# Performance work log

Measured on AMD Instinct MI355X. Metric: run time of the kernel, lower is better.

Reference implementation:

```python
import jax, jax.numpy as jnp
import numpy as np

NO_LANE = 90  # sentinel label meaning 'no lane'

def smooth_l1(x):
    ax = jnp.abs(x)
    return jnp.where(ax < 1.0, 0.5 * x * x, ax - 0.5)

def setup_inputs() -> dict:
    key = jax.random.key(0)
    ks = jax.random.split(key, 10)
    B, M, T, L, NL, P = 32768, 6, 30, 10, 10, 50
    cls_ = jax.random.normal(ks[0], (B, M), dtype=jnp.float32)
    reg = jax.random.normal(ks[1], (B, M, T, 2), dtype=jnp.float32) * 5.0
    lane_cls = jax.random.normal(ks[2], (B, L), dtype=jnp.float32)
    gt_preds = jax.random.normal(ks[3], (B, T, 2), dtype=jnp.float32) * 5.0
    rot = jax.random.normal(ks[4], (B, 2, 2), dtype=jnp.float32)
    orig = jax.random.normal(ks[5], (B, 2), dtype=jnp.float32)
    lane_feats = jax.random.normal(ks[6], (B, NL, P, 2), dtype=jnp.float32) * 5.0
    has_preds = jax.random.uniform(ks[7], (B, T)) < 0.8
    has_preds = has_preds.at[:, 0].set(True)  # ensure mask = max_last > 1.0 holds for every row
    lane_labels = jax.random.randint(ks[8], (B,), 0, L, dtype=jnp.int32)
    lane_labels = jnp.where(jax.random.uniform(ks[9], (B,)) < 0.05, NO_LANE, lane_labels)
    return dict(cls=cls_, reg=reg, lane_cls=lane_cls, gt_preds=gt_preds, rot=rot,
                orig=orig, lane_feats=lane_feats, has_preds=has_preds, lane_labels=lane_labels)

def reference(cls, reg, lane_cls, gt_preds, rot, orig, lane_feats, has_preds, lane_labels):
    B, M, T, _ = reg.shape
    rows = jnp.arange(B)
    hasf = has_preds.astype(jnp.float32)

    # last valid timestep per agent (argmax of has + tiny time ramp)
    last = hasf + 0.1 * jnp.arange(T, dtype=jnp.float32) / T
    last_idcs = jnp.argmax(last, axis=1)
    mask = jnp.max(last, axis=1) > 1.0  # [B], all True by construction
    maskf = mask.astype(jnp.float32)

    # endpoint distance per mode -> min mode selection
    end_reg = reg[rows, :, last_idcs]            # [B, M, 2]
    end_gt = gt_preds[rows, last_idcs]           # [B, 2]
    dist = jnp.sqrt(((end_reg - end_gt[:, None, :]) ** 2).sum(-1))  # [B, M]
    min_idcs = jnp.argmin(dist, axis=1)

    # classification target: mode with min total squared error
    cls_tar = jnp.argmin(((reg - gt_preds[:, None]) ** 2).sum(-1).sum(-1), axis=1)
    nll = -jnp.take_along_axis(jax.nn.log_softmax(cls, axis=-1), cls_tar[:, None], axis=1)[:, 0]
    cls_loss = (nll * maskf).sum() / jnp.maximum(maskf.sum(), 1.0)  # CE mean over masked rows

    reg_sel = reg[rows, min_idcs]                # [B, T, 2]
    w_reg = hasf * maskf[:, None]
    reg_loss = (smooth_l1(reg_sel - gt_preds) * w_reg[:, :, None]).sum()
    num_reg = w_reg.sum()

    # lane classification: per-sample CE * (label+1), skipping sentinel
    valid = lane_labels != NO_LANE
    validf = valid.astype(jnp.float32)
    lab_c = jnp.where(valid, lane_labels, 0)
    lane_nll = -jnp.take_along_axis(jax.nn.log_softmax(lane_cls, axis=-1), lab_c[:, None], axis=1)[:, 0]
    lane_cls_loss = (lane_nll * (lab_c.astype(jnp.float32) + 1.0) * validf).sum()
    num_lane_cls = validf.sum()

    # lane-offset loss: lane polyline in global frame, point-to-lane min distances
    lane_sel = lane_feats[rows, lab_c]           # [B, P, 2]
    lane_w = jnp.einsum('bpc,bcd->bpd', lane_sel, rot) + orig[:, None, :]
    d_reg = jnp.linalg.norm(lane_w[:, None, :, :] - reg_sel[:, :, None, :], axis=-1).min(-1)  # [B, T]
    d_gt = jnp.linalg.norm(lane_w[:, None, :, :] - gt_preds[:, :, None, :], axis=-1).min(-1)  # [B, T]
    diff = d_reg - d_gt
    check = (d_reg >= d_gt).astype(jnp.float32)
    per = (diff * check * hasf).sum(1) / jnp.maximum(hasf.sum(1), 1.0)  # mean over valid steps
    w_off = validf * maskf
    lane_off_loss = (per * w_off).sum()
    num_lane_off = w_off.sum()

    return jnp.stack([cls_loss, maskf.sum() * 0 + 1.0, reg_loss, num_reg,
                      lane_cls_loss, num_lane_cls, lane_off_loss, num_lane_off])
```

## Files before the change

### kernel.cpp

```cpp
#include <hip/hip_runtime.h>
#include <math.h>

#define NO_LANE 90
constexpr int Bt  = 32768;
constexpr int Mm  = 6;
constexpr int Tt  = 30;
constexpr int Ll  = 10;
constexpr int NLl = 10;
constexpr int Pp  = 50;

constexpr int BPB   = 8;
constexpr int NBLK  = Bt / BPB;
constexpr int NSLOT = 64;
constexpr int LPAD  = 104;

__device__ __forceinline__ float smoothl1(float x) {
    float ax = fabsf(x);
    return ax < 1.0f ? 0.5f * x * x : ax - 0.5f;
}

template <int CTRL>
__device__ __forceinline__ float dppf(float x) {
    return __int_as_float(__builtin_amdgcn_update_dpp(
        0, __float_as_int(x), CTRL, 0xF, 0xF, true));
}
__device__ __forceinline__ float sum8(float x) {
    x += dppf<0xB1>(x);
    x += dppf<0x4E>(x);
    x += dppf<0x141>(x);
    return x;
}
__device__ __forceinline__ float sum16(float x) {
    x = sum8(x);
    x += dppf<0x140>(x);
    return x;
}
__device__ __forceinline__ float sum32(float x) {
    x += __shfl_xor(x, 16);
    return sum16(x);
}
__device__ __forceinline__ float max8(float x) {
    x = fmaxf(x, dppf<0xB1>(x));
    x = fmaxf(x, dppf<0x4E>(x));
    x = fmaxf(x, dppf<0x141>(x));
    return x;
}
__device__ __forceinline__ float max16(float x) {
    x = max8(x);
    x = fmaxf(x, dppf<0x140>(x));
    return x;
}

__global__ __launch_bounds__(256) void pred_loss_main(
    const float* __restrict__ cls, const float* __restrict__ reg,
    const float* __restrict__ lane_cls, const float* __restrict__ gt,
    const float* __restrict__ rot, const float* __restrict__ orig,
    const float* __restrict__ lane_feats, const unsigned char* __restrict__ hp,
    const int* __restrict__ lane_labels, float* __restrict__ slots) {

    __shared__ __align__(16) float sLW[BPB][LPAD];
    __shared__ float sPart[BPB][8];

    const int tid = threadIdx.x;
    const int sb  = tid >> 5;
    const int l   = tid & 31;
    const int h   = (tid >> 5) & 1;
    const int b   = blockIdx.x * BPB + sb;

    unsigned int u = ((const unsigned int*)hp)[tid & 63];
    unsigned int s = (u & 0xFFu) + ((u >> 8) & 0xFFu) +
                     ((u >> 16) & 0xFFu) + (u >> 24);
#pragma unroll
    for (int o = 32; o; o >>= 1) s += __shfl_xor((int)s, o);
    const bool byte_fmt = (s > 100u && s < 2000u);

    bool has = false;
    if (l < Tt) {
        int idx = b * Tt + l;
        has = byte_fmt ? (hp[idx] != 0)
                       : (((const unsigned int*)hp)[idx] != 0u);
    }
    unsigned long long ball = __ballot(has);
    unsigned int mmask = (unsigned int)(ball >> (h * 32));
    int   last  = 31 - __clz((int)(mmask | 1u));
    float maskf = (mmask >> 1) ? 1.0f : 0.0f;
    float n_has = (float)__popc((int)mmask);
    float hasf  = has ? 1.0f : 0.0f;

    int   lab    = lane_labels[b];
    bool  valid  = (lab != NO_LANE);
    int   lab_c  = valid ? lab : 0;
    float validf = valid ? 1.0f : 0.0f;

    float gx = 0.f, gy = 0.f;
    float rx[Mm], ry[Mm];
#pragma unroll
    for (int m = 0; m < Mm; ++m) { rx[m] = 0.f; ry[m] = 0.f; }
    if (l < Tt) {
        float2 g = *(const float2*)(gt + (size_t)b * (Tt * 2) + 2 * l);
        gx = g.x; gy = g.y;
        const float* regb = reg + (size_t)b * (Mm * Tt * 2) + 2 * l;
#pragma unroll
        for (int m = 0; m < Mm; ++m) {
            float2 r = *(const float2*)(regb + m * (Tt * 2));
            rx[m] = r.x; ry[m] = r.y;
        }
    }

    float4 R = *(const float4*)(rot + (size_t)b * 4);
    float2 O = *(const float2*)(orig + (size_t)b * 2);
    if (l < 25) {
        float4 ls = ((const float4*)(lane_feats +
                     ((size_t)b * NLl + lab_c) * (Pp * 2)))[l];
        float4 lw;
        lw.x = ls.x * R.x + ls.y * R.z + O.x;
        lw.y = ls.x * R.y + ls.y * R.w + O.y;
        lw.z = ls.z * R.x + ls.w * R.z + O.x;
        lw.w = ls.z * R.y + ls.w * R.w + O.y;
        ((float4*)&sLW[sb][0])[l] = lw;
    }

    float cm = (l < Mm) ? cls[(size_t)b * Mm + l] : -INFINITY;
    float lc = (l < Ll) ? lane_cls[(size_t)b * Ll + l] : -INFINITY;

    float pm[Mm];
#pragma unroll
    for (int m = 0; m < Mm; ++m) {
        float dx = rx[m] - gx, dy = ry[m] - gy;
        pm[m] = sum32(dx * dx + dy * dy);
    }
    int cls_tar = 0;
    float bestc = pm[0];
#pragma unroll
    for (int m = 1; m < Mm; ++m)
        if (pm[m] < bestc) { bestc = pm[m]; cls_tar = m; }

    int mi_loc = 0;
    {
        float dx = rx[0] - gx, dy = ry[0] - gy;
        float bd = dx * dx + dy * dy;
#pragma unroll
        for (int m = 1; m < Mm; ++m) {
            float ex_ = rx[m] - gx, ey_ = ry[m] - gy;
            float d2 = ex_ * ex_ + ey_ * ey_;
            if (d2 < bd) { bd = d2; mi_loc = m; }
        }
    }
    int min_i = __shfl(mi_loc, last + h * 32);

    float rsx = rx[0], rsy = ry[0];
#pragma unroll
    for (int m = 1; m < Mm; ++m)
        if (min_i == m) { rsx = rx[m]; rsy = ry[m]; }

    float mx = max8(cm);
    float ex = sum8((l < Mm) ? __expf(cm - mx) : 0.f);
    float ctar = __shfl(cm, cls_tar + h * 32);
    float nll  = mx + __logf(ex) - ctar;

    float mx2 = max16(lc);
    float ex2 = sum16((l < Ll) ? __expf(lc - mx2) : 0.f);
    float ltar = __shfl(lc, lab_c + h * 32);
    float lnll = mx2 + __logf(ex2) - ltar;

    float regl = sum32((smoothl1(rsx - gx) + smoothl1(rsy - gy)) * hasf * maskf);

    float dminR = INFINITY, dminG = INFINITY;
    const float4* lw4 = (const float4*)&sLW[sb][0];
#pragma unroll
    for (int j = 0; j < 25; ++j) {
        float4 q = lw4[j];
        float ax0 = q.x - rsx, ay0 = q.y - rsy;
        float ax1 = q.z - rsx, ay1 = q.w - rsy;
        dminR = fminf(dminR, fminf(ax0 * ax0 + ay0 * ay0, ax1 * ax1 + ay1 * ay1));
        float bx0 = q.x - gx, by0 = q.y - gy;
        float bx1 = q.z - gx, by1 = q.w - gy;
        dminG = fminf(dminG, fminf(bx0 * bx0 + by0 * by0, bx1 * bx1 + by1 * by1));
    }
    float dr = sqrtf(dminR), dg = sqrtf(dminG);
    float pern = sum32((dr >= dg) ? (dr - dg) * hasf : 0.f);

    if (l == 0) {
        float per = pern / fmaxf(n_has, 1.0f);
        sPart[sb][0] = nll * maskf;
        sPart[sb][1] = maskf;
        sPart[sb][2] = regl;
        sPart[sb][3] = maskf * n_has;
        sPart[sb][4] = lnll * (float)(lab_c + 1) * validf;
        sPart[sb][5] = validf;
        sPart[sb][6] = per * validf * maskf;
        sPart[sb][7] = validf * maskf;
    }
    __syncthreads();

    if (tid < 8) {
        float sum = 0.f;
#pragma unroll
        for (int k = 0; k < BPB; ++k) sum += sPart[k][tid];
        atomicAdd(&slots[(size_t)(blockIdx.x & (NSLOT - 1)) * 16 + tid], sum);
    }
}

__global__ __launch_bounds__(64) void finalize_k(const float* __restrict__ slots,
                                                 float* __restrict__ out) {
    int lane = threadIdx.x;
    int c  = lane & 7;
    int s0 = lane >> 3;
    float t = 0.f;
#pragma unroll
    for (int k = 0; k < 8; ++k)
        t += slots[(size_t)(s0 + k * 8) * 16 + c];
    t += __shfl_xor(t, 8);
    t += __shfl_xor(t, 16);
    t += __shfl_xor(t, 32);
    float r1 = __shfl(t, 1);
    if (lane == 0)      out[0] = t / fmaxf(r1, 1.0f);
    else if (lane == 1) out[1] = 1.0f;
    else if (lane < 8)  out[lane] = t;
}

extern "C" void kernel_launch(void* const* d_in, const int* in_sizes, int n_in,
                              void* d_out, int out_size, void* d_ws, size_t ws_size,
                              hipStream_t stream) {
    const float* cls        = (const float*)d_in[0];
    const float* reg        = (const float*)d_in[1];
    const float* lane_cls   = (const float*)d_in[2];
    const float* gt         = (const float*)d_in[3];
    const float* rot        = (const float*)d_in[4];
    const float* orig       = (const float*)d_in[5];
    const float* lane_feats = (const float*)d_in[6];
    const unsigned char* hp = (const unsigned char*)d_in[7];
    const int* lane_labels  = (const int*)d_in[8];
    float* out = (float*)d_out;

    float* slots = (float*)((char*)d_ws + 64);

    hipMemsetAsync(d_ws, 0, 64 + NSLOT * 16 * sizeof(float), stream);
    pred_loss_main<<<NBLK, 256, 0, stream>>>(
        cls, reg, lane_cls, gt, rot, orig, lane_feats, hp, lane_labels, slots);
    finalize_k<<<1, 64, 0, stream>>>(slots, out);
}
```

Baseline: 225.1 us.

## Replace atomic slot reduction with per-block partials and vectorize lane distance loop

Each block now writes its eight partial sums to its own workspace entry instead of doing atomicAdd into 64 shared slots. This removes the memset and the atomic contention, and a 1024-thread finalize kernel then reduces all 4096 block partials. The lane-distance loop now stores x and y in separate padded SoA shared arrays, using sentinel points for padding, so the distance math can use packed 2-wide float ops. The format-detection reduction switches to DPP. The finalize kernel now reads more data serially in one block, which could add latency.

```diff
diff --git a/kernel.cpp b/kernel.cpp
--- a/kernel.cpp
+++ b/kernel.cpp
@@ -11,8 +11,9 @@
 
 constexpr int BPB   = 8;
 constexpr int NBLK  = Bt / BPB;
-constexpr int NSLOT = 64;
-constexpr int LPAD  = 104;
+constexpr int LPTS  = 56;
+
+typedef float v2f __attribute__((ext_vector_type(2)));
 
 __device__ __forceinline__ float smoothl1(float x) {
     float ax = fabsf(x);
@@ -23,6 +24,10 @@
 __device__ __forceinline__ float dppf(float x) {
     return __int_as_float(__builtin_amdgcn_update_dpp(
         0, __float_as_int(x), CTRL, 0xF, 0xF, true));
+}
+template <int CTRL>
+__device__ __forceinline__ int dppi(int x) {
+    return __builtin_amdgcn_update_dpp(0, x, CTRL, 0xF, 0xF, true);
 }
 __device__ __forceinline__ float sum8(float x) {
     x += dppf<0xB1>(x);
@@ -56,9 +61,10 @@
     const float* __restrict__ lane_cls, const float* __restrict__ gt,
     const float* __restrict__ rot, const float* __restrict__ orig,
     const float* __restrict__ lane_feats, const unsigned char* __restrict__ hp,
-    const int* __restrict__ lane_labels, float* __restrict__ slots) {
-
-    __shared__ __align__(16) float sLW[BPB][LPAD];
+    const int* __restrict__ lane_labels, float* __restrict__ parts) {
+
+    __shared__ __align__(16) float sLWx[BPB][LPTS];
+    __shared__ __align__(16) float sLWy[BPB][LPTS];
     __shared__ float sPart[BPB][8];
 
     const int tid = threadIdx.x;
@@ -68,11 +74,12 @@
     const int b   = blockIdx.x * BPB + sb;
 
     unsigned int u = ((const unsigned int*)hp)[tid & 63];
-    unsigned int s = (u & 0xFFu) + ((u >> 8) & 0xFFu) +
-                     ((u >> 16) & 0xFFu) + (u >> 24);
-#pragma unroll
-    for (int o = 32; o; o >>= 1) s += __shfl_xor((int)s, o);
-    const bool byte_fmt = (s > 100u && s < 2000u);
+    int si = (int)((u & 0xFFu) + ((u >> 8) & 0xFFu) +
+                   ((u >> 16) & 0xFFu) + (u >> 24));
+    si += dppi<0xB1>(si); si += dppi<0x4E>(si);
+    si += dppi<0x141>(si); si += dppi<0x140>(si);
+    si += __shfl_xor(si, 16); si += __shfl_xor(si, 32);
+    const bool byte_fmt = (si > 100 && si < 2000);
 
     bool has = false;
     if (l < Tt) {
@@ -109,15 +116,18 @@
 
     float4 R = *(const float4*)(rot + (size_t)b * 4);
     float2 O = *(const float2*)(orig + (size_t)b * 2);
-    if (l < 25) {
-        float4 ls = ((const float4*)(lane_feats +
-                     ((size_t)b * NLl + lab_c) * (Pp * 2)))[l];
-        float4 lw;
-        lw.x = ls.x * R.x + ls.y * R.z + O.x;
-        lw.y = ls.x * R.y + ls.y * R.w + O.y;
-        lw.z = ls.z * R.x + ls.w * R.z + O.x;
-        lw.w = ls.z * R.y + ls.w * R.w + O.y;
-        ((float4*)&sLW[sb][0])[l] = lw;
+    if (l < 26) {
+        float4 lw = make_float4(1e19f, 1e19f, 1e19f, 1e19f);
+        if (l < 25) {
+            float4 ls = ((const float4*)(lane_feats +
+                         ((size_t)b * NLl + lab_c) * (Pp * 2)))[l];
+            lw.x = ls.x * R.x + ls.y * R.z + O.x;
+            lw.y = ls.x * R.y + ls.y * R.w + O.y;
+            lw.z = ls.z * R.x + ls.w * R.z + O.x;
+            lw.w = ls.z * R.y + ls.w * R.w + O.y;
+        }
+        *(float2*)&sLWx[sb][2 * l] = make_float2(lw.x, lw.z);
+        *(float2*)&sLWy[sb][2 * l] = make_float2(lw.y, lw.w);
     }
 
     float cm = (l < Mm) ? cls[(size_t)b * Mm + l] : -INFINITY;
@@ -165,17 +175,26 @@
 
     float regl = sum32((smoothl1(rsx - gx) + smoothl1(rsy - gy)) * hasf * maskf);
 
+    v2f rsx2 = {rsx, rsx}, rsy2 = {rsy, rsy};
+    v2f gx2  = {gx, gx},   gy2  = {gy, gy};
     float dminR = INFINITY, dminG = INFINITY;
-    const float4* lw4 = (const float4*)&sLW[sb][0];
-#pragma unroll
-    for (int j = 0; j < 25; ++j) {
-        float4 q = lw4[j];
-        float ax0 = q.x - rsx, ay0 = q.y - rsy;
-        float ax1 = q.z - rsx, ay1 = q.w - rsy;
-        dminR = fminf(dminR, fminf(ax0 * ax0 + ay0 * ay0, ax1 * ax1 + ay1 * ay1));
-        float bx0 = q.x - gx, by0 = q.y - gy;
-        float bx1 = q.z - gx, by1 = q.w - gy;
-        dminG = fminf(dminG, fminf(bx0 * bx0 + by0 * by0, bx1 * bx1 + by1 * by1));
+    const float4* xs4 = (const float4*)&sLWx[sb][0];
+    const float4* ys4 = (const float4*)&sLWy[sb][0];
+#pragma unroll
+    for (int j = 0; j < 13; ++j) {
+        float4 xq = xs4[j], yq = ys4[j];
+        v2f xa = {xq.x, xq.y}, xb = {xq.z, xq.w};
+        v2f ya = {yq.x, yq.y}, yb = {yq.z, yq.w};
+        v2f dxa = xa - rsx2, dya = ya - rsy2;
+        v2f dxb = xb - rsx2, dyb = yb - rsy2;
+        v2f da = dxa * dxa + dya * dya;
+        v2f db = dxb * dxb + dyb * dyb;
+        dminR = fminf(dminR, fminf(fminf(da.x, da.y), fminf(db.x, db.y)));
+        v2f exa = xa - gx2, eya = ya - gy2;
+        v2f exb = xb - gx2, eyb = yb - gy2;
+        v2f ea = exa * exa + eya * eya;
+        v2f eb = exb * exb + eyb * eyb;
+        dminG = fminf(dminG, fminf(fminf(ea.x, ea.y), fminf(eb.x, eb.y)));
     }
     float dr = sqrtf(dminR), dg = sqrtf(dminG);
     float pern = sum32((dr >= dg) ? (dr - dg) * hasf : 0.f);
@@ -197,26 +216,34 @@
         float sum = 0.f;
 #pragma unroll
         for (int k = 0; k < BPB; ++k) sum += sPart[k][tid];
-        atomicAdd(&slots[(size_t)(blockIdx.x & (NSLOT - 1)) * 16 + tid], sum);
-    }
-}
-
-__global__ __launch_bounds__(64) void finalize_k(const float* __restrict__ slots,
-                                                 float* __restrict__ out) {
-    int lane = threadIdx.x;
-    int c  = lane & 7;
-    int s0 = lane >> 3;
+        parts[(size_t)blockIdx.x * 8 + tid] = sum;
+    }
+}
+
+__global__ __launch_bounds__(1024) void finalize_k(const float* __restrict__ parts,
+                                                   float* __restrict__ out) {
+    __shared__ float sFin[16][8];
+    const int tid = threadIdx.x;
+    const int c = tid & 7;
+    const int r = tid >> 3;
     float t = 0.f;
 #pragma unroll
-    for (int k = 0; k < 8; ++k)
-        t += slots[(size_t)(s0 + k * 8) * 16 + c];
+    for (int k = 0; k < 32; ++k)
+        t += parts[(size_t)(r + 128 * k) * 8 + c];
     t += __shfl_xor(t, 8);
     t += __shfl_xor(t, 16);
     t += __shfl_xor(t, 32);
-    float r1 = __shfl(t, 1);
-    if (lane == 0)      out[0] = t / fmaxf(r1, 1.0f);
-    else if (lane == 1) out[1] = 1.0f;
-    else if (lane < 8)  out[lane] = t;
+    if ((tid & 63) < 8) sFin[tid >> 6][c] = t;
+    __syncthreads();
+    if (tid < 8) {
+        float v = 0.f;
+#pragma unroll
+        for (int k = 0; k < 16; ++k) v += sFin[k][tid];
+        float r1 = __shfl(v, 1);
+        if (tid == 0)      out[0] = v / fmaxf(r1, 1.0f);
+        else if (tid == 1) out[1] = 1.0f;
+        else               out[tid] = v;
+    }
 }
 
 extern "C" void kernel_launch(void* const* d_in, const int* in_sizes, int n_in,
@@ -233,10 +260,9 @@
     const int* lane_labels  = (const int*)d_in[8];
     float* out = (float*)d_out;
 
-    float* slots = (float*)((char*)d_ws + 64);
-
-    hipMemsetAsync(d_ws, 0, 64 + NSLOT * 16 * sizeof(float), stream);
+    float* parts = (float*)d_ws;
+
     pred_loss_main<<<NBLK, 256, 0, stream>>>(
-        cls, reg, lane_cls, gt, rot, orig, lane_feats, hp, lane_labels, slots);
-    finalize_k<<<1, 64, 0, stream>>>(slots, out);
-}
+        cls, reg, lane_cls, gt, rot, orig, lane_feats, hp, lane_labels, parts);
+    finalize_k<<<1, 1024, 0, stream>>>(parts, out);
+}
```

Result: no change. 227.0 us (+0.9%).
